# Optimization experiments

Hardware: AMD Instinct MI355X
Metric: run time of the kernel (lower is better)

## Reference

```python
import jax, jax.numpy as jnp
import numpy as np

DIM = 256
HEADS = 8
WS = 7          # window size
SS = 3          # shift size
B = 16
HIMG = 56
WIMG = 56
N = WS * WS     # tokens per window = 49
HID = DIM * 4


def _rel_index(ws):
    coords = np.stack(np.meshgrid(np.arange(ws), np.arange(ws), indexing='ij')).reshape(2, -1)
    rel = (coords[:, :, None] - coords[:, None, :]).transpose(1, 2, 0)
    rel[:, :, 0] += ws - 1
    rel[:, :, 1] += ws - 1
    rel[:, :, 0] *= 2 * ws - 1
    return rel.sum(-1)  # (N, N) int

REL_IDX = jnp.asarray(_rel_index(WS))


def _make_attn_mask(H, W, ws, ss):
    img = np.zeros((H, W), dtype=np.float32)
    cnt = 0
    for hs in (slice(0, -ws), slice(-ws, -ss), slice(-ss, None)):
        for wsl in (slice(0, -ws), slice(-ws, -ss), slice(-ss, None)):
            img[hs, wsl] = cnt
            cnt += 1
    mw = img.reshape(H // ws, ws, W // ws, ws).transpose(0, 2, 1, 3).reshape(-1, ws * ws)
    diff = mw[:, None, :] - mw[:, :, None]  # (nW, N, N)
    return jnp.asarray(np.where(diff != 0, -100.0, 0.0).astype(np.float32))


def _layernorm(x, g, b):
    m = jnp.mean(x, -1, keepdims=True)
    v = jnp.mean((x - m) ** 2, -1, keepdims=True)
    return (x - m) / jnp.sqrt(v + 1e-5) * g + b


def _win_part(x, ws):
    Bb, H, W, C = x.shape
    x = x.reshape(Bb, H // ws, ws, W // ws, ws, C).transpose(0, 1, 3, 2, 4, 5)
    return x.reshape(-1, ws * ws, C)  # (B*nW, N, C)


def _win_rev(w, ws, H, W):
    C = w.shape[-1]
    Bb = w.shape[0] // ((H // ws) * (W // ws))
    x = w.reshape(Bb, H // ws, W // ws, ws, ws, C).transpose(0, 1, 3, 2, 4, 5)
    return x.reshape(Bb, H, W, C)


def setup_inputs() -> dict:
    key = jax.random.key(0)
    ks = jax.random.split(key, 20)
    n = lambda k, s, sc=0.02: jax.random.normal(k, s, dtype=jnp.float32) * sc
    inp = {
        'x1': jax.random.normal(ks[0], (B, HIMG * WIMG, DIM), dtype=jnp.float32),
        'x2': jax.random.normal(ks[1], (B, HIMG * WIMG, DIM), dtype=jnp.float32),
        'x3': jax.random.normal(ks[2], (B, HIMG * WIMG, DIM), dtype=jnp.float32),
        'attn_mask': _make_attn_mask(HIMG, WIMG, WS, SS),
        'g1': jnp.ones((DIM,), jnp.float32), 'bb1': jnp.zeros((DIM,), jnp.float32),
        'wq': n(ks[3], (DIM, DIM)), 'bq': jnp.zeros((DIM,), jnp.float32),
        'wk': n(ks[4], (DIM, DIM)), 'bk': jnp.zeros((DIM,), jnp.float32),
        'wv': n(ks[5], (DIM, DIM)), 'bv': jnp.zeros((DIM,), jnp.float32),
        'rel_table': n(ks[6], ((2 * WS - 1) ** 2, HEADS)),
        'wp': n(ks[7], (DIM, DIM)), 'bp': jnp.zeros((DIM,), jnp.float32),
        'g2': jnp.ones((DIM,), jnp.float32), 'bb2': jnp.zeros((DIM,), jnp.float32),
        'fw1': n(ks[8], (DIM, HID)), 'fb1': jnp.zeros((HID,), jnp.float32),
        'fw2': n(ks[9], (HID, DIM)), 'fb2': jnp.zeros((DIM,), jnp.float32),
        'H': HIMG, 'W': WIMG,
    }
    return inp


def reference(x1, x2, x3, attn_mask, g1, bb1, wq, bq, wk, bk, wv, bv, rel_table,
              wp, bp, g2, bb2, fw1, fb1, fw2, fb2, H, W):
    Bb, L, C = x1.shape
    hd = C // HEADS
    shortcut = x1

    def prep(x):
        x = _layernorm(x, g1, bb1).reshape(Bb, H, W, C)
        return jnp.roll(x, (-SS, -SS), axis=(1, 2))  # cyclic shift (shift_size>0)

    xw1 = _win_part(prep(x1), WS)  # (B*nW, N, C)
    xw2 = _win_part(prep(x2), WS)
    xw3 = _win_part(prep(x3), WS)

    def to_heads(x, w, b):
        y = x @ w + b
        return y.reshape(-1, N, HEADS, hd).transpose(0, 2, 1, 3)  # (B_, h, N, hd)

    q = to_heads(xw1, wq, bq) * (hd ** -0.5)
    k = to_heads(xw2, wk, bk)
    v = to_heads(xw3, wv, bv)

    attn = jnp.einsum('bhnd,bhmd->bhnm', q, k)  # (B_, h, N, N)
    bias = rel_table[REL_IDX].transpose(2, 0, 1)  # (h, N, N) gather
    attn = attn + bias[None]
    nW = attn_mask.shape[0]
    attn = attn.reshape(Bb, nW, HEADS, N, N) + attn_mask[None, :, None]
    attn = jax.nn.softmax(attn.reshape(-1, HEADS, N, N), axis=-1)

    out = jnp.einsum('bhnm,bhmd->bhnd', attn, v).transpose(0, 2, 1, 3).reshape(-1, N, C)
    out = out @ wp + bp

    x = _win_rev(out, WS, H, W)
    x = jnp.roll(x, (SS, SS), axis=(1, 2)).reshape(Bb, L, C)  # reverse shift

    x = shortcut + x
    h = jax.nn.gelu(_layernorm(x, g2, bb2) @ fw1 + fb1, approximate=False) @ fw2 + fb2
    return x + h
```

## Files before the change

kernel.cpp:

```cpp
#include <hip/hip_runtime.h>

typedef unsigned short u16;
typedef short bf16x8 __attribute__((ext_vector_type(8)));
typedef float f32x4 __attribute__((ext_vector_type(4)));

__device__ __forceinline__ u16 f2bf(float f) {
  union { float f; unsigned u; } x; x.f = f;
  unsigned r = x.u + 0x7FFFu + ((x.u >> 16) & 1u);
  return (u16)(r >> 16);
}
__device__ __forceinline__ float bf2f(u16 u) {
  union { unsigned u; float f; } x; x.u = (unsigned)u << 16; return x.f;
}
__device__ __forceinline__ float gelu_f(float x) {
  float t = 0.7978845608028654f * x * (1.f + 0.044715f * x * x);
  return x / (1.f + __expf(-2.f * t));
}
__device__ __forceinline__ void gll16(const void* g, void* l) {
  __builtin_amdgcn_global_load_lds(
      (const __attribute__((address_space(1))) unsigned int*)g,
      (__attribute__((address_space(3))) unsigned int*)l, 16, 0, 0);
}
__device__ __forceinline__ size_t winmap(int t) {
  int win = t / 49, i = t - win * 49;
  int b = win >> 6, wi = win & 63;
  int ih = i / 7, iw = i - ih * 7;
  int h2 = (wi >> 3) * 7 + ih + 3; if (h2 >= 56) h2 -= 56;
  int w2 = (wi & 7) * 7 + iw + 3; if (w2 >= 56) w2 -= 56;
  return ((size_t)b * 3136 + (size_t)h2 * 56 + w2) * 256;
}

__global__ __launch_bounds__(256)
void prep_all(const float* __restrict__ wq, const float* __restrict__ wk,
              const float* __restrict__ wv, const float* __restrict__ wp,
              const float* __restrict__ fw1, const float* __restrict__ fw2,
              u16* __restrict__ wqt, u16* __restrict__ wkt,
              u16* __restrict__ wvt, u16* __restrict__ wpt,
              u16* __restrict__ fw1t, u16* __restrict__ fw2t,
              const float* __restrict__ rel, const float* __restrict__ mask,
              float* __restrict__ Bp) {
  const int bx = blockIdx.x;
  const int tid = threadIdx.x;
  if (bx >= 192) {
    const int blk = bx - 192;
    const int wi = blk >> 3, h = blk & 7;
    const float* mrow = mask + (size_t)wi * 2401;
    float* ob = Bp + (size_t)blk * 4096;
#pragma unroll
    for (int e = 0; e < 16; ++e) {
      int pos = e * 256 + tid;
      int r = pos & 3, lane = (pos >> 2) & 63, mini = pos >> 8;
      int mi = mini >> 2, ni = mini & 3;
      int row = mi * 16 + (lane >> 4) * 4 + r;
      int col = ni * 16 + (lane & 15);
      float val;
      if (col >= 49) val = -1e30f;
      else if (row >= 49) val = 0.f;
      else {
        int idx = (row / 7 - col / 7 + 6) * 13 + (row % 7 - col % 7 + 6);
        val = rel[idx * 8 + h] + mrow[row * 49 + col];
      }
      ob[pos] = val;
    }
    return;
  }
  const float* in; u16* out; int K, N, t;
  if (bx < 64) {
    int j = bx >> 4; t = bx & 15; K = 256; N = 256;
    in = j == 0 ? wq : (j == 1 ? wk : (j == 2 ? wv : wp));
    out = j == 0 ? wqt : (j == 1 ? wkt : (j == 2 ? wvt : wpt));
  } else if (bx < 128) {
    t = bx - 64; in = fw1; out = fw1t; K = 256; N = 1024;
  } else {
    t = bx - 128; in = fw2; out = fw2t; K = 1024; N = 256;
  }
  const int ntn = N >> 6;
  const int tk = t / ntn, tn = t - tk * ntn;
  __shared__ u16 tile[64][72];
#pragma unroll
  for (int it = 0; it < 4; ++it) {
    int G = it * 256 + tid;
    int kk = G >> 4, gg = G & 15;
    float4 v = *(const float4*)(in + (size_t)(tk * 64 + kk) * N + tn * 64 + gg * 4);
    tile[kk][gg * 4 + 0] = f2bf(v.x);
    tile[kk][gg * 4 + 1] = f2bf(v.y);
    tile[kk][gg * 4 + 2] = f2bf(v.z);
    tile[kk][gg * 4 + 3] = f2bf(v.w);
  }
  __syncthreads();
#pragma unroll
  for (int it = 0; it < 4; ++it) {
    int G = it * 256 + tid;
    int nn = G >> 4, gk = G & 15;
    ushort4 o;
    o.x = tile[gk * 4 + 0][nn];
    o.y = tile[gk * 4 + 1][nn];
    o.z = tile[gk * 4 + 2][nn];
    o.w = tile[gk * 4 + 3][nn];
    *(ushort4*)(out + (size_t)(tn * 64 + nn) * K + tk * 64 + gk * 4) = o;
  }
}

__global__ __launch_bounds__(256, 4)
void gemm_qkv(const float* __restrict__ X0, const float* __restrict__ X1,
              const float* __restrict__ X2, const float* __restrict__ lng,
              const float* __restrict__ lnb, const u16* __restrict__ Bt,
              const float* __restrict__ b0, const float* __restrict__ b1,
              const float* __restrict__ b2, float alpha,
              u16* __restrict__ out_) {
  __shared__ __align__(16) u16 Bl[2][32 * 256];
  const int tid = threadIdx.x, lane = tid & 63, wave = tid >> 6;
  const int q = lane >> 4, m = lane & 15;
  const int wm = wave >> 1, wn = wave & 1;
  const int y = blockIdx.y;
  const size_t aoff = (size_t)y * 12845056;
  Bt += (size_t)y * 65536;
  const float* bias = (y == 0) ? b0 : (y == 1 ? b1 : b2);
  const float al = (y == 0) ? alpha : 1.f;
  const float* xsrc = (y == 0) ? X0 : (y == 1 ? X1 : X2);
  const long rowBase = (long)blockIdx.x * 64;

  bf16x8 af[2][8];
  {
    u16* Abuf = (u16*)Bl;
    const float4 gv = *(const float4*)(lng + lane * 4);
    const float4 bv = *(const float4*)(lnb + lane * 4);
#pragma unroll
    for (int pp = 0; pp < 16; ++pp) {
      int lrow = wave * 16 + pp;
      size_t src = winmap((int)(rowBase + lrow));
      float4 v = *(const float4*)(xsrc + src + lane * 4);
      float sm = v.x + v.y + v.z + v.w;
      float s2 = v.x * v.x + v.y * v.y + v.z * v.z + v.w * v.w;
#pragma unroll
      for (int d = 32; d > 0; d >>= 1) {
        sm += __shfl_xor(sm, d);
        s2 += __shfl_xor(s2, d);
      }
      float mean = sm * (1.f / 256.f);
      float rstd = rsqrtf(s2 * (1.f / 256.f) - mean * mean + 1e-5f);
      ushort4 ov;
      ov.x = f2bf((v.x - mean) * rstd * gv.x + bv.x);
      ov.y = f2bf((v.y - mean) * rstd * gv.y + bv.y);
      ov.z = f2bf((v.z - mean) * rstd * gv.z + bv.z);
      ov.w = f2bf((v.w - mean) * rstd * gv.w + bv.w);
      int g = lane >> 1;
      int gs = (g & ~7) | ((g & 7) ^ (lrow & 7));
      *(ushort4*)&Abuf[lrow * 256 + gs * 8 + (lane & 1) * 4] = ov;
    }
    __syncthreads();
#pragma unroll
    for (int mt = 0; mt < 2; ++mt) {
      int row = wm * 32 + mt * 16 + m;
#pragma unroll
      for (int ks = 0; ks < 8; ++ks) {
        int g = ks * 4 + q;
        int gs = (g & ~7) | ((g & 7) ^ (row & 7));
        af[mt][ks] = *(const bf16x8*)&Abuf[row * 256 + gs * 8];
      }
    }
    __syncthreads();
  }

  auto stageB = [&](u16* dst, int c) {
#pragma unroll
    for (int it = 0; it < 4; ++it) {
      int G = it * 256 + tid;
      int r = G >> 5, g = G & 31;
      int gs = (g & ~7) | ((g & 7) ^ (r & 7));
      gll16(Bt + (size_t)c * 8192 + r * 256 + gs * 8, dst + G * 8);
    }
  };

  stageB(Bl[0], 0);

  for (int c = 0; c < 8; ++c) {
    __syncthreads();
    if (c + 1 < 8) stageB(Bl[(c + 1) & 1], c + 1);
    const u16* Bc = Bl[c & 1];

    f32x4 acc[2] = {};
    const int rb = wn * 16 + m;
#pragma unroll
    for (int ks = 0; ks < 8; ++ks) {
      int g = ks * 4 + q;
      int gs = (g & ~7) | ((g & 7) ^ (rb & 7));
      bf16x8 bfv = *(const bf16x8*)&Bc[rb * 256 + gs * 8];
      acc[0] = __builtin_amdgcn_mfma_f32_16x16x32_bf16(af[0][ks], bfv, acc[0], 0, 0, 0);
      acc[1] = __builtin_amdgcn_mfma_f32_16x16x32_bf16(af[1][ks], bfv, acc[1], 0, 0, 0);
    }

    const int colb = c * 32 + wn * 16 + m;
    const float bvv = bias[colb];
    u16* out = out_ + aoff;
#pragma unroll
    for (int mt = 0; mt < 2; ++mt) {
      size_t rw = (size_t)(rowBase + wm * 32 + mt * 16 + q * 4) * 256;
#pragma unroll
      for (int r = 0; r < 4; ++r) {
        float vv = (acc[mt][r] + bvv) * al;
        out[rw + (size_t)r * 256 + colb] = f2bf(vv);
      }
    }
  }
}

__global__ __launch_bounds__(256, 2)
void proj_mlp(const u16* __restrict__ attn_o, const u16* __restrict__ wpt,
              const float* __restrict__ bpj, const float* __restrict__ x1,
              const float* __restrict__ g2, const float* __restrict__ bb2,
              const u16* __restrict__ fw1t, const float* __restrict__ fb1,
              const u16* __restrict__ fw2t, const float* __restrict__ fb2,
              float* __restrict__ out) {
  __shared__ __align__(16) u16 xbuf[64 * 256];
  __shared__ __align__(16) u16 Bd0[32 * 256];
  __shared__ __align__(16) u16 Bd1[256 * 32];
  __shared__ __align__(16) u16 slab[4][16 * 32];
  const int tid = threadIdx.x, lane = tid & 63, wave = tid >> 6;
  const int q = lane >> 4, m = lane & 15;
  const long rowBase = (long)blockIdx.x * 64;

  size_t obaseP[4];
#pragma unroll
  for (int r = 0; r < 4; ++r)
    obaseP[r] = winmap((int)(rowBase + wave * 16 + q * 4 + r));

  bf16x8 afP[8];
  {
    const u16* ap = attn_o + (size_t)(rowBase + wave * 16 + m) * 256 + q * 8;
#pragma unroll
    for (int ks = 0; ks < 8; ++ks) afP[ks] = *(const bf16x8*)(ap + ks * 32);
  }

  auto stageW = [&](int c, u16* dst) {
    const u16* src = wpt + (size_t)c * 8192;
#pragma unroll
    for (int it = 0; it < 4; ++it) {
      int G = it * 256 + tid;
      int r = G >> 5, g = G & 31;
      int gs = (g & ~7) | ((g & 7) ^ (r & 7));
      gll16(src + r * 256 + gs * 8, dst + G * 8);
    }
  };
  auto stageB1 = [&](int hc) {
    const u16* src = fw1t + (size_t)hc * 8192;
#pragma unroll
    for (int it = 0; it < 4; ++it) {
      int G = it * 256 + tid;
      int r = G >> 5, g = G & 31;
      int gs = (g & ~7) | ((g & 7) ^ (r & 7));
      gll16(src + r * 256 + gs * 8, Bd0 + G * 8);
    }
  };
  auto stageB2 = [&](int hc) {
#pragma unroll
    for (int it = 0; it < 4; ++it) {
      int G = it * 256 + tid;
      int n = G >> 2, g = G & 3;
      int gs = g ^ ((n >> 1) & 3);
      gll16(fw2t + (size_t)n * 1024 + hc * 32 + gs * 8, Bd1 + G * 8);
    }
  };

  stageW(0, Bd0);
  for (int c = 0; c < 8; ++c) {
    __syncthreads();
    if (c + 1 < 8) stageW(c + 1, (c & 1) ? Bd0 : Bd1);
    const u16* Bc = (c & 1) ? Bd1 : Bd0;

    f32x4 acc1[2] = {};
#pragma unroll
    for (int ks = 0; ks < 8; ++ks) {
      int g = ks * 4 + q;
      bf16x8 bfv[2];
#pragma unroll
      for (int nt = 0; nt < 2; ++nt) {
        int rb = nt * 16 + m;
        int gs = (g & ~7) | ((g & 7) ^ (rb & 7));
        bfv[nt] = *(const bf16x8*)&Bc[rb * 256 + gs * 8];
      }
#pragma unroll
      for (int nt = 0; nt < 2; ++nt)
        acc1[nt] = __builtin_amdgcn_mfma_f32_16x16x32_bf16(afP[ks], bfv[nt], acc1[nt], 0, 0, 0);
    }
#pragma unroll
    for (int nt = 0; nt < 2; ++nt) {
      int col = c * 32 + nt * 16 + m;
      float bvv = bpj[col];
      int g = col >> 3;
#pragma unroll
      for (int r = 0; r < 4; ++r) {
        int row = wave * 16 + q * 4 + r;
        float v = acc1[nt][r] + bvv + x1[obaseP[r] + col];
        int gs = (g & ~7) | ((g & 7) ^ (row & 7));
        xbuf[row * 256 + gs * 8 + (col & 7)] = f2bf(v);
      }
    }
  }
  stageB1(0);

  float meanK = 0.f, rstdK = 0.f;
#pragma unroll
  for (int rr = 0; rr < 16; ++rr) {
    int row = wave * 16 + rr;
    ushort4 xv = *(const ushort4*)&xbuf[row * 256 + lane * 4];
    float a0 = bf2f(xv.x), a1 = bf2f(xv.y), a2 = bf2f(xv.z), a3 = bf2f(xv.w);
    float s = a0 + a1 + a2 + a3;
    float s2 = a0 * a0 + a1 * a1 + a2 * a2 + a3 * a3;
#pragma unroll
    for (int d = 32; d > 0; d >>= 1) {
      s += __shfl_xor(s, d);
      s2 += __shfl_xor(s2, d);
    }
    float mean = s * (1.f / 256.f);
    float rstd = rsqrtf(s2 * (1.f / 256.f) - mean * mean + 1e-5f);
    if ((lane & 15) == rr) { meanK = mean; rstdK = rstd; }
  }
  bf16x8 af[8];
  {
    int row = wave * 16 + m;
#pragma unroll
    for (int ks = 0; ks < 8; ++ks) {
      int g = ks * 4 + q;
      int gs = (g & ~7) | ((g & 7) ^ (row & 7));
      bf16x8 xv = *(const bf16x8*)&xbuf[row * 256 + gs * 8];
      float4 ga = *(const float4*)(g2 + ks * 32 + q * 8);
      float4 gb = *(const float4*)(g2 + ks * 32 + q * 8 + 4);
      float4 ba = *(const float4*)(bb2 + ks * 32 + q * 8);
      float4 bb = *(const float4*)(bb2 + ks * 32 + q * 8 + 4);
      bf16x8 o;
      o[0] = (short)f2bf((bf2f((u16)xv[0]) - meanK) * rstdK * ga.x + ba.x);
      o[1] = (short)f2bf((bf2f((u16)xv[1]) - meanK) * rstdK * ga.y + ba.y);
      o[2] = (short)f2bf((bf2f((u16)xv[2]) - meanK) * rstdK * ga.z + ba.z);
      o[3] = (short)f2bf((bf2f((u16)xv[3]) - meanK) * rstdK * ga.w + ba.w);
      o[4] = (short)f2bf((bf2f((u16)xv[4]) - meanK) * rstdK * gb.x + bb.x);
      o[5] = (short)f2bf((bf2f((u16)xv[5]) - meanK) * rstdK * gb.y + bb.y);
      o[6] = (short)f2bf((bf2f((u16)xv[6]) - meanK) * rstdK * gb.z + bb.z);
      o[7] = (short)f2bf((bf2f((u16)xv[7]) - meanK) * rstdK * gb.w + bb.w);
      af[ks] = o;
    }
  }

  f32x4 accO[16] = {};
  u16* sl = slab[wave];

  for (int hc = 0; hc < 32; ++hc) {
    __syncthreads();
    stageB2(hc);

    f32x4 acc1[2] = {};
#pragma unroll
    for (int ks = 0; ks < 8; ++ks) {
      int g = ks * 4 + q;
      bf16x8 bfv[2];
#pragma unroll
      for (int nt = 0; nt < 2; ++nt) {
        int r = nt * 16 + m;
        int gs = (g & ~7) | ((g & 7) ^ (r & 7));
        bfv[nt] = *(const bf16x8*)&Bd0[r * 256 + gs * 8];
      }
#pragma unroll
      for (int nt = 0; nt < 2; ++nt)
        acc1[nt] = __builtin_amdgcn_mfma_f32_16x16x32_bf16(af[ks], bfv[nt], acc1[nt], 0, 0, 0);
    }
#pragma unroll
    for (int nt = 0; nt < 2; ++nt) {
      float b1 = fb1[hc * 32 + nt * 16 + m];
      int gcol = nt * 2 + (m >> 3);
#pragma unroll
      for (int r = 0; r < 4; ++r) {
        int row = q * 4 + r;
        float h = gelu_f(acc1[nt][r] + b1);
        int gs = gcol ^ ((row >> 1) & 3);
        sl[row * 32 + gs * 8 + (m & 7)] = f2bf(h);
      }
    }
    __syncthreads();
    if (hc + 1 < 32) stageB1(hc + 1);

    {
      int gsa = q ^ ((m >> 1) & 3);
      bf16x8 pa = *(const bf16x8*)&sl[m * 32 + gsa * 8];
#pragma unroll
      for (int nt = 0; nt < 16; ++nt) {
        int n = nt * 16 + m;
        int gs2 = q ^ ((n >> 1) & 3);
        bf16x8 bv2 = *(const bf16x8*)&Bd1[n * 32 + gs2 * 8];
        accO[nt] = __builtin_amdgcn_mfma_f32_16x16x32_bf16(pa, bv2, accO[nt], 0, 0, 0);
      }
    }
  }

#pragma unroll
  for (int nt = 0; nt < 16; ++nt) {
    int col = nt * 16 + m;
    float b2 = fb2[col];
    int g = col >> 3;
#pragma unroll
    for (int r = 0; r < 4; ++r) {
      int row = wave * 16 + q * 4 + r;
      int gs = (g & ~7) | ((g & 7) ^ (row & 7));
      float xv = bf2f(xbuf[row * 256 + gs * 8 + (col & 7)]);
      out[obaseP[r] + col] = xv + accO[nt][r] + b2;
    }
  }
}

__global__ __launch_bounds__(64)
void attn_mfma(const u16* __restrict__ q, const u16* __restrict__ k,
               const u16* __restrict__ v, const float* __restrict__ Bp,
               u16* __restrict__ out) {
  __shared__ u16 Pl[64 * 64];
  __shared__ u16 VT[32 * 64];
  const int lane = threadIdx.x;
  const int unit = blockIdx.x;
  const int win = unit >> 3, head = unit & 7;
  const size_t base = (size_t)win * 49 * 256 + head * 32;

  {
    const int key = lane;
    const u16* vp = v + base + (size_t)key * 256;
#pragma unroll
    for (int p = 0; p < 4; ++p) {
      bf16x8 vv = {};
      if (key < 49) vv = *(const bf16x8*)(vp + p * 8);
#pragma unroll
      for (int e = 0; e < 8; ++e) {
        int dim = p * 8 + e;
        int sw = (dim ^ (dim >> 3)) & 7;
        VT[dim * 64 + ((((key >> 3) ^ sw) << 3) | (key & 7))] = (u16)vv[e];
      }
    }
  }

  const f32x4* bp = (const f32x4*)(Bp + (size_t)((win & 63) * 8 + head) * 4096);
  f32x4 acc[4][4];
#pragma unroll
  for (int mi = 0; mi < 4; ++mi)
#pragma unroll
    for (int ni = 0; ni < 4; ++ni)
      acc[mi][ni] = bp[(mi * 4 + ni) * 64 + lane];

  bf16x8 qf[4], kf[4];
#pragma unroll
  for (int mi = 0; mi < 4; ++mi)
    qf[mi] = *(const bf16x8*)(q + base + (size_t)(mi * 16 + (lane & 15)) * 256 + (lane >> 4) * 8);
#pragma unroll
  for (int ni = 0; ni < 4; ++ni)
    kf[ni] = *(const bf16x8*)(k + base + (size_t)(ni * 16 + (lane & 15)) * 256 + (lane >> 4) * 8);

#pragma unroll
  for (int mi = 0; mi < 4; ++mi)
#pragma unroll
    for (int ni = 0; ni < 4; ++ni)
      acc[mi][ni] = __builtin_amdgcn_mfma_f32_16x16x32_bf16(qf[mi], kf[ni], acc[mi][ni], 0, 0, 0);

  float rinv[4][4];
#pragma unroll
  for (int mi = 0; mi < 4; ++mi) {
#pragma unroll
    for (int r = 0; r < 4; ++r) {
      float mx = fmaxf(fmaxf(acc[mi][0][r], acc[mi][1][r]),
                       fmaxf(acc[mi][2][r], acc[mi][3][r]));
#pragma unroll
      for (int off = 1; off < 16; off <<= 1) mx = fmaxf(mx, __shfl_xor(mx, off));
      float s = 0.f;
#pragma unroll
      for (int ni = 0; ni < 4; ++ni) {
        float e = __expf(acc[mi][ni][r] - mx);
        acc[mi][ni][r] = e;
        s += e;
      }
#pragma unroll
      for (int off = 1; off < 16; off <<= 1) s += __shfl_xor(s, off);
      rinv[mi][r] = 1.f / s;
    }
  }

#pragma unroll
  for (int mi = 0; mi < 4; ++mi)
#pragma unroll
    for (int ni = 0; ni < 4; ++ni)
#pragma unroll
      for (int r = 0; r < 4; ++r) {
        int row = mi * 16 + (lane >> 4) * 4 + r;
        int col = ni * 16 + (lane & 15);
        int sw = (row ^ (row >> 3)) & 7;
        Pl[row * 64 + ((((col >> 3) ^ sw) << 3) | (col & 7))] = f2bf(acc[mi][ni][r]);
      }

  f32x4 acc2[4][2] = {};
#pragma unroll
  for (int ks = 0; ks < 2; ++ks) {
    bf16x8 pa[4], vb[2];
#pragma unroll
    for (int mi = 0; mi < 4; ++mi) {
      int row = mi * 16 + (lane & 15);
      int sw = (row ^ (row >> 3)) & 7;
      pa[mi] = *(const bf16x8*)&Pl[row * 64 + (((ks * 4 + (lane >> 4)) ^ sw) << 3)];
    }
#pragma unroll
    for (int n2 = 0; n2 < 2; ++n2) {
      int dim = n2 * 16 + (lane & 15);
      int sw = (dim ^ (dim >> 3)) & 7;
      vb[n2] = *(const bf16x8*)&VT[dim * 64 + (((ks * 4 + (lane >> 4)) ^ sw) << 3)];
    }
#pragma unroll
    for (int mi = 0; mi < 4; ++mi)
#pragma unroll
      for (int n2 = 0; n2 < 2; ++n2)
        acc2[mi][n2] = __builtin_amdgcn_mfma_f32_16x16x32_bf16(pa[mi], vb[n2], acc2[mi][n2], 0, 0, 0);
  }

#pragma unroll
  for (int mi = 0; mi < 4; ++mi)
#pragma unroll
    for (int r = 0; r < 4; ++r) {
      int row = mi * 16 + (lane >> 4) * 4 + r;
      if (row < 49) {
        float rv = rinv[mi][r];
#pragma unroll
        for (int n2 = 0; n2 < 2; ++n2) {
          int col = n2 * 16 + (lane & 15);
          out[base + (size_t)row * 256 + col] = f2bf(acc2[mi][n2][r] * rv);
        }
      }
    }
}

extern "C" void kernel_launch(void* const* d_in, const int* in_sizes, int n_in,
                              void* d_out, int out_size, void* d_ws, size_t ws_size,
                              hipStream_t stream) {
  const float* x1 = (const float*)d_in[0];
  const float* x2 = (const float*)d_in[1];
  const float* x3 = (const float*)d_in[2];
  const float* amask = (const float*)d_in[3];
  const float* g1 = (const float*)d_in[4];
  const float* bb1 = (const float*)d_in[5];
  const float* wq = (const float*)d_in[6];
  const float* bq = (const float*)d_in[7];
  const float* wk = (const float*)d_in[8];
  const float* bk = (const float*)d_in[9];
  const float* wv = (const float*)d_in[10];
  const float* bvb = (const float*)d_in[11];
  const float* rel = (const float*)d_in[12];
  const float* wp = (const float*)d_in[13];
  const float* bp = (const float*)d_in[14];
  const float* g2 = (const float*)d_in[15];
  const float* bb2 = (const float*)d_in[16];
  const float* fw1 = (const float*)d_in[17];
  const float* fb1 = (const float*)d_in[18];
  const float* fw2 = (const float*)d_in[19];
  const float* fb2 = (const float*)d_in[20];

  char* wsb = (char*)d_ws;
  const size_t S = (size_t)50176 * 256 * 2;
  u16* attn_o = (u16*)(wsb + 0 * S);
  u16* qb = (u16*)(wsb + 3 * S);
  u16* kbuf = (u16*)(wsb + 4 * S);
  u16* vbuf = (u16*)(wsb + 5 * S);
  u16* wqt = (u16*)(wsb + 6 * S);
  u16* wkt = wqt + 65536;
  u16* wvt = wkt + 65536;
  u16* wpt = wvt + 65536;
  u16* fw1t = wpt + 65536;
  u16* fw2t = fw1t + 262144;
  float* Bp = (float*)(fw2t + 262144);

  prep_all<<<dim3(704), 256, 0, stream>>>(wq, wk, wv, wp, fw1, fw2, wqt, wkt,
                                          wvt, wpt, fw1t, fw2t, rel, amask, Bp);

  gemm_qkv<<<dim3(784, 3), 256, 0, stream>>>(
      x1, x2, x3, g1, bb1, wqt, bq, bk, bvb, 0.17677669529663687f, qb);

  attn_mfma<<<dim3(8192), 64, 0, stream>>>(qb, kbuf, vbuf, Bp, attn_o);

  proj_mlp<<<dim3(784), 256, 0, stream>>>(attn_o, wpt, bp, x1, g2, bb2,
                                          fw1t, fb1, fw2t, fb2,
                                          (float*)d_out);
}
```

Baseline: 257.9 us.

## Keep residual in packed registers and alias LDS to raise proj_mlp occupancy

proj_mlp now keeps the projected residual as packed bf16 pairs in registers, computes the LayerNorm statistics from those registers with lane shuffles, and stages rows through a single aliased shared buffer that reuses the weight staging space. This shrinks LDS from about 69KB to about 37KB, and the launch bound goes from 2 to 3 blocks per CU to raise occupancy. The trade-off is 32 extra registers held live through the MLP loop under a tighter register budget, which risks spills, plus extra barriers around the aliased buffer.

```diff
diff --git a/kernel.cpp b/kernel.cpp
--- a/kernel.cpp
+++ b/kernel.cpp
@@ -11,6 +11,15 @@
 }
 __device__ __forceinline__ float bf2f(u16 u) {
   union { unsigned u; float f; } x; x.u = (unsigned)u << 16; return x.f;
+}
+__device__ __forceinline__ float bf_lo(unsigned u) {
+  union { unsigned u; float f; } x; x.u = u << 16; return x.f;
+}
+__device__ __forceinline__ float bf_hi(unsigned u) {
+  union { unsigned u; float f; } x; x.u = u & 0xFFFF0000u; return x.f;
+}
+__device__ __forceinline__ unsigned pack2bf(float a, float b) {
+  return (unsigned)f2bf(a) | ((unsigned)f2bf(b) << 16);
 }
 __device__ __forceinline__ float gelu_f(float x) {
   float t = 0.7978845608028654f * x * (1.f + 0.044715f * x * x);
@@ -205,25 +214,20 @@
   }
 }
 
-__global__ __launch_bounds__(256, 2)
+__global__ __launch_bounds__(256, 3)
 void proj_mlp(const u16* __restrict__ attn_o, const u16* __restrict__ wpt,
               const float* __restrict__ bpj, const float* __restrict__ x1,
               const float* __restrict__ g2, const float* __restrict__ bb2,
               const u16* __restrict__ fw1t, const float* __restrict__ fb1,
               const u16* __restrict__ fw2t, const float* __restrict__ fb2,
               float* __restrict__ out) {
-  __shared__ __align__(16) u16 xbuf[64 * 256];
-  __shared__ __align__(16) u16 Bd0[32 * 256];
-  __shared__ __align__(16) u16 Bd1[256 * 32];
-  __shared__ __align__(16) u16 slab[4][16 * 32];
+  __shared__ __align__(16) u16 sm[18432];
+  u16* Bd0 = sm;
+  u16* Bd1 = sm + 8192;
+  u16* slabs = sm + 16384;
   const int tid = threadIdx.x, lane = tid & 63, wave = tid >> 6;
   const int q = lane >> 4, m = lane & 15;
   const long rowBase = (long)blockIdx.x * 64;
-
-  size_t obaseP[4];
-#pragma unroll
-  for (int r = 0; r < 4; ++r)
-    obaseP[r] = winmap((int)(rowBase + wave * 16 + q * 4 + r));
 
   bf16x8 afP[8];
   {
@@ -262,60 +266,99 @@
     }
   };
 
-  stageW(0, Bd0);
-  for (int c = 0; c < 8; ++c) {
-    __syncthreads();
-    if (c + 1 < 8) stageW(c + 1, (c & 1) ? Bd0 : Bd1);
-    const u16* Bc = (c & 1) ? Bd1 : Bd0;
-
-    f32x4 acc1[2] = {};
-#pragma unroll
-    for (int ks = 0; ks < 8; ++ks) {
-      int g = ks * 4 + q;
-      bf16x8 bfv[2];
+  unsigned xp[32];
+  {
+    size_t obaseP[4];
+#pragma unroll
+    for (int r = 0; r < 4; ++r)
+      obaseP[r] = winmap((int)(rowBase + wave * 16 + q * 4 + r));
+
+    stageW(0, Bd0);
+    for (int c = 0; c < 8; ++c) {
+      __syncthreads();
+      if (c + 1 < 8) stageW(c + 1, (c & 1) ? Bd0 : Bd1);
+      const u16* Bc = (c & 1) ? Bd1 : Bd0;
+
+      f32x4 acc1[2] = {};
+#pragma unroll
+      for (int ks = 0; ks < 8; ++ks) {
+        int g = ks * 4 + q;
+        bf16x8 bfv[2];
+#pragma unroll
+        for (int nt = 0; nt < 2; ++nt) {
+          int rb = nt * 16 + m;
+          int gs = (g & ~7) | ((g & 7) ^ (rb & 7));
+          bfv[nt] = *(const bf16x8*)&Bc[rb * 256 + gs * 8];
+        }
+#pragma unroll
+        for (int nt = 0; nt < 2; ++nt)
+          acc1[nt] = __builtin_amdgcn_mfma_f32_16x16x32_bf16(afP[ks], bfv[nt], acc1[nt], 0, 0, 0);
+      }
 #pragma unroll
       for (int nt = 0; nt < 2; ++nt) {
-        int rb = nt * 16 + m;
-        int gs = (g & ~7) | ((g & 7) ^ (rb & 7));
-        bfv[nt] = *(const bf16x8*)&Bc[rb * 256 + gs * 8];
-      }
+        int col = c * 32 + nt * 16 + m;
+        float bvv = bpj[col];
+        float v0 = acc1[nt][0] + bvv + x1[obaseP[0] + col];
+        float v1 = acc1[nt][1] + bvv + x1[obaseP[1] + col];
+        float v2 = acc1[nt][2] + bvv + x1[obaseP[2] + col];
+        float v3 = acc1[nt][3] + bvv + x1[obaseP[3] + col];
+        xp[c * 4 + nt * 2 + 0] = pack2bf(v0, v1);
+        xp[c * 4 + nt * 2 + 1] = pack2bf(v2, v3);
+      }
+    }
+  }
+
+  float meanK, rstdK;
+  {
+    float s[4] = {}, s2[4] = {};
+#pragma unroll
+    for (int c = 0; c < 8; ++c)
 #pragma unroll
       for (int nt = 0; nt < 2; ++nt)
-        acc1[nt] = __builtin_amdgcn_mfma_f32_16x16x32_bf16(afP[ks], bfv[nt], acc1[nt], 0, 0, 0);
-    }
-#pragma unroll
-    for (int nt = 0; nt < 2; ++nt) {
-      int col = c * 32 + nt * 16 + m;
-      float bvv = bpj[col];
-      int g = col >> 3;
-#pragma unroll
-      for (int r = 0; r < 4; ++r) {
-        int row = wave * 16 + q * 4 + r;
-        float v = acc1[nt][r] + bvv + x1[obaseP[r] + col];
-        int gs = (g & ~7) | ((g & 7) ^ (row & 7));
-        xbuf[row * 256 + gs * 8 + (col & 7)] = f2bf(v);
-      }
-    }
-  }
-  stageB1(0);
-
-  float meanK = 0.f, rstdK = 0.f;
-#pragma unroll
-  for (int rr = 0; rr < 16; ++rr) {
-    int row = wave * 16 + rr;
-    ushort4 xv = *(const ushort4*)&xbuf[row * 256 + lane * 4];
-    float a0 = bf2f(xv.x), a1 = bf2f(xv.y), a2 = bf2f(xv.z), a3 = bf2f(xv.w);
-    float s = a0 + a1 + a2 + a3;
-    float s2 = a0 * a0 + a1 * a1 + a2 * a2 + a3 * a3;
-#pragma unroll
-    for (int d = 32; d > 0; d >>= 1) {
-      s += __shfl_xor(s, d);
-      s2 += __shfl_xor(s2, d);
-    }
-    float mean = s * (1.f / 256.f);
-    float rstd = rsqrtf(s2 * (1.f / 256.f) - mean * mean + 1e-5f);
-    if ((lane & 15) == rr) { meanK = mean; rstdK = rstd; }
-  }
+#pragma unroll
+        for (int rp = 0; rp < 2; ++rp) {
+          unsigned p = xp[c * 4 + nt * 2 + rp];
+          float a = bf_lo(p), b = bf_hi(p);
+          s[rp * 2] += a; s2[rp * 2] += a * a;
+          s[rp * 2 + 1] += b; s2[rp * 2 + 1] += b * b;
+        }
+#pragma unroll
+    for (int r = 0; r < 4; ++r) {
+#pragma unroll
+      for (int d = 1; d < 16; d <<= 1) {
+        s[r] += __shfl_xor(s[r], d);
+        s2[r] += __shfl_xor(s2[r], d);
+      }
+    }
+    float ms = (m & 2) ? ((m & 1) ? s[3] : s[2]) : ((m & 1) ? s[1] : s[0]);
+    float qs = (m & 2) ? ((m & 1) ? s2[3] : s2[2]) : ((m & 1) ? s2[1] : s2[0]);
+    float msel = __shfl(ms, (m >> 2) * 16 + m);
+    float qsel = __shfl(qs, (m >> 2) * 16 + m);
+    meanK = msel * (1.f / 256.f);
+    rstdK = rsqrtf(qsel * (1.f / 256.f) - meanK * meanK + 1e-5f);
+  }
+
+  __syncthreads();
+  {
+#pragma unroll
+    for (int c = 0; c < 8; ++c)
+#pragma unroll
+      for (int nt = 0; nt < 2; ++nt) {
+        int col = c * 32 + nt * 16 + m;
+        int g = col >> 3;
+#pragma unroll
+        for (int rp = 0; rp < 2; ++rp) {
+          unsigned p = xp[c * 4 + nt * 2 + rp];
+          int row0 = wave * 16 + q * 4 + rp * 2;
+          int gs0 = (g & ~7) | ((g & 7) ^ (row0 & 7));
+          sm[row0 * 256 + gs0 * 8 + (col & 7)] = (u16)(p & 0xFFFF);
+          int row1 = row0 + 1;
+          int gs1 = (g & ~7) | ((g & 7) ^ (row1 & 7));
+          sm[row1 * 256 + gs1 * 8 + (col & 7)] = (u16)(p >> 16);
+        }
+      }
+  }
+  __syncthreads();
   bf16x8 af[8];
   {
     int row = wave * 16 + m;
@@ -323,7 +366,7 @@
     for (int ks = 0; ks < 8; ++ks) {
       int g = ks * 4 + q;
       int gs = (g & ~7) | ((g & 7) ^ (row & 7));
-      bf16x8 xv = *(const bf16x8*)&xbuf[row * 256 + gs * 8];
+      bf16x8 xv = *(const bf16x8*)&sm[row * 256 + gs * 8];
       float4 ga = *(const float4*)(g2 + ks * 32 + q * 8);
       float4 gb = *(const float4*)(g2 + ks * 32 + q * 8 + 4);
       float4 ba = *(const float4*)(bb2 + ks * 32 + q * 8);
@@ -340,9 +383,11 @@
       af[ks] = o;
     }
   }
+  __syncthreads();
+  stageB1(0);
 
   f32x4 accO[16] = {};
-  u16* sl = slab[wave];
+  u16* sl = slabs + wave * 512;
 
   for (int hc = 0; hc < 32; ++hc) {
     __syncthreads();
@@ -391,17 +436,21 @@
     }
   }
 
-#pragma unroll
-  for (int nt = 0; nt < 16; ++nt) {
-    int col = nt * 16 + m;
-    float b2 = fb2[col];
-    int g = col >> 3;
-#pragma unroll
-    for (int r = 0; r < 4; ++r) {
-      int row = wave * 16 + q * 4 + r;
-      int gs = (g & ~7) | ((g & 7) ^ (row & 7));
-      float xv = bf2f(xbuf[row * 256 + gs * 8 + (col & 7)]);
-      out[obaseP[r] + col] = xv + accO[nt][r] + b2;
+  {
+    size_t obaseP[4];
+#pragma unroll
+    for (int r = 0; r < 4; ++r)
+      obaseP[r] = winmap((int)(rowBase + wave * 16 + q * 4 + r));
+#pragma unroll
+    for (int nt = 0; nt < 16; ++nt) {
+      int col = nt * 16 + m;
+      float b2 = fb2[col];
+      unsigned p0 = xp[(nt >> 1) * 4 + (nt & 1) * 2 + 0];
+      unsigned p1 = xp[(nt >> 1) * 4 + (nt & 1) * 2 + 1];
+      out[obaseP[0] + col] = bf_lo(p0) + accO[nt][0] + b2;
+      out[obaseP[1] + col] = bf_hi(p0) + accO[nt][1] + b2;
+      out[obaseP[2] + col] = bf_lo(p1) + accO[nt][2] + b2;
+      out[obaseP[3] + col] = bf_hi(p1) + accO[nt][3] + b2;
     }
   }
 }
```

New measurement: 310.6 us. 1.2x slower.
